# Performance work log

Hardware: AMD Instinct MI355X
Metric: run time of the kernel (lower is better)

## Reference

```python
import jax, jax.numpy as jnp
import numpy as np

B, L, C, K, NLEV, VOCAB, OUT = 32, 1024, 512, 2, 4, 128, 11


def setup_inputs() -> dict:
    key = jax.random.key(0)
    ks = jax.random.split(key, 8)
    x = jax.random.randint(ks[0], (B, L), 0, VOCAB, dtype=jnp.int32)
    mask = jax.random.randint(ks[1], (B, L), 0, 2).astype(jnp.bool_)
    emb = jax.random.uniform(ks[2], (VOCAB, C), minval=-0.5, maxval=0.5, dtype=jnp.float32)
    w1 = jax.random.normal(ks[3], (NLEV, C, C, K), dtype=jnp.float32) * 0.02
    b1 = jnp.zeros((NLEV, C), dtype=jnp.float32)
    w2 = jax.random.normal(ks[4], (NLEV, C, C, K), dtype=jnp.float32) * 0.02
    b2 = jnp.zeros((NLEV, C), dtype=jnp.float32)
    dec_w = jax.random.uniform(ks[5], (OUT, C), minval=-0.5, maxval=0.5, dtype=jnp.float32)
    dec_b = jnp.zeros((OUT,), dtype=jnp.float32)
    return dict(x=x, mask=mask, emb=emb, w1=w1, b1=b1, w2=w2, b2=b2, dec_w=dec_w, dec_b=dec_b)


def _causal_conv(h, w, b, dilation):
    # h: [B, C, L], w: [Cout, Cin, K]; left-pad (K-1)*d == conv+chomp in TCN
    pad = (w.shape[-1] - 1) * dilation
    out = jax.lax.conv_general_dilated(
        h, w, window_strides=(1,), padding=[(pad, 0)],
        rhs_dilation=(dilation,), dimension_numbers=("NCH", "OIH", "NCH"))
    return out + b[None, :, None]


def reference(x, mask, emb, w1, b1, w2, b2, dec_w, dec_b):
    h = emb[x].transpose(0, 2, 1)  # [B, C, L]
    for i in range(NLEV):  # fixed small number of TCN levels
        d = 2 ** i
        res = h
        h = jax.nn.relu(_causal_conv(h, w1[i], b1[i], d))
        h = jax.nn.relu(_causal_conv(h, w2[i], b2[i], d))
        h = jax.nn.relu(h + res)  # residual (in==out channels -> identity shortcut)
    y = jnp.einsum("bcl,oc->blo", h, dec_w) + dec_b  # [B, L, OUT]
    # mask-gather: original keeps only mask-true positions; zero others (jit-safe)
    return y * mask[..., None].astype(y.dtype)
```

## Files before the change

### kernel.cpp

```cpp
#include <hip/hip_runtime.h>
#include <stdint.h>

#define BB 32
#define LL 1024
#define CC 512
#define NN (BB * LL)
#define NLEVS 4
#define OUTD 11
#define LPAD 8
#define LROWS (LL + LPAD)

typedef __attribute__((ext_vector_type(8))) short bf16x8;
typedef __attribute__((ext_vector_type(4))) float f32x4;

static __device__ __forceinline__ unsigned short f2bf(float f) {
    union { float f; uint32_t u; } v; v.f = f;
    uint32_t u = v.u;
    uint32_t r = (u + 0x7fffu + ((u >> 16) & 1u)) >> 16;
    return (unsigned short)r;
}
static __device__ __forceinline__ float bf2f(unsigned short h) {
    union { uint32_t u; float f; } v; v.u = ((uint32_t)h) << 16;
    return v.f;
}

static __device__ __forceinline__ void llds16(const unsigned short* g, unsigned short* l) {
    __builtin_amdgcn_global_load_lds(
        (const __attribute__((address_space(1))) unsigned int*)g,
        (__attribute__((address_space(3))) unsigned int*)l, 16, 0, 0);
}

__global__ __launch_bounds__(256) void prep_kernel(
    const int* __restrict__ x, const float* __restrict__ emb,
    const float* __restrict__ w1, const float* __restrict__ w2,
    const float* __restrict__ dw,
    unsigned short* __restrict__ Hb0, unsigned short* __restrict__ Hb1,
    unsigned short* __restrict__ WpT, unsigned short* __restrict__ dwp)
{
    int b = blockIdx.x;
    if (b < 16384) {
        int e = b * 256 + threadIdx.x;
        int cv = e >> 19;
        int r = e & 524287;
        int j = r >> 12;
        int co = (r >> 3) & 511;
        int h = r & 7;
        int kidx = j * 8 + h;
        int k = (kidx < 512) ? 1 : 0;
        int ci = kidx & 511;
        int lvl = cv >> 1;
        const float* w = (cv & 1) ? w2 : w1;
        WpT[e] = f2bf(w[(((size_t)(lvl * 512 + co) * 512) + ci) * 2 + k]);
    } else if (b < 24576) {
        int t = (b - 16384) * 256 + threadIdx.x;
        int n = t >> 6;
        int c8 = (t & 63) * 8;
        int idx = x[n];
        const float* src = emb + (size_t)idx * CC + c8;
        float4 v0 = *(const float4*)src;
        float4 v1 = *(const float4*)(src + 4);
        ushort4 a, bb;
        a.x = f2bf(v0.x); a.y = f2bf(v0.y); a.z = f2bf(v0.z); a.w = f2bf(v0.w);
        bb.x = f2bf(v1.x); bb.y = f2bf(v1.y); bb.z = f2bf(v1.z); bb.w = f2bf(v1.w);
        int prow = (n >> 10) * LROWS + LPAD + (n & (LL - 1));
        unsigned short* dst = Hb0 + (size_t)prow * CC + c8;
        *(ushort4*)dst = a;
        *(ushort4*)(dst + 4) = bb;
    } else if (b < 24704) {
        int t = (b - 24576) * 256 + threadIdx.x;
        unsigned short* base = (t >> 14) ? Hb1 : Hb0;
        int rem = t & 16383;
        int p = rem >> 9;
        int q = rem & 511;
        size_t off = (size_t)p * (LROWS * CC) + (size_t)q * 8;
        *(uint4*)(base + off) = (uint4){0u, 0u, 0u, 0u};
    } else {
        int e = (b - 24704) * 256 + threadIdx.x;
        int jb = e >> 7;
        int o = (e >> 3) & 15;
        int j = e & 7;
        dwp[e] = f2bf((o < OUTD) ? dw[o * CC + jb * 8 + j] : 0.f);
    }
}

#define BUFH (17 * 512)
template <bool HAS_RES>
__global__ __launch_bounds__(256, 4) void conv_gemm(
    const unsigned short* __restrict__ Ain, const unsigned short* __restrict__ WpT,
    const float* __restrict__ bias, const unsigned short* __restrict__ resB,
    unsigned short* __restrict__ OutB, int d)
{
    __shared__ unsigned short sA[2 * BUFH];
    __shared__ int s_ready[8];
    __shared__ int s_done[8];

    const int tid = threadIdx.x;
    const int wave = tid >> 6, lane = tid & 63;

    const int bid = blockIdx.x;
    const int xcd = bid & 7;
    const int local = bid >> 3;
    const int cb = local >> 5;
    const int nb = xcd + 8 * (local & 31);
    const int co0 = cb * 128;
    const int n0 = nb * 128;

    const int rbase = (n0 >> 10) * LROWS + LPAD + (n0 & (LL - 1));
    const int wm = (wave >> 1) * 64;
    const int wn = (wave & 1) * 64;
    const int lm = lane & 15, quad = lane >> 4;

    const int r8 = lane >> 3;
    const int c8 = lane & 7;

    if (tid < 8) { s_ready[tid] = 0; s_done[tid] = 0; }
    __syncthreads();

    f32x4 acc[4][4];
#pragma unroll
    for (int i = 0; i < 4; ++i)
#pragma unroll
        for (int j = 0; j < 4; ++j) acc[i][j] = (f32x4){0.f, 0.f, 0.f, 0.f};

    auto issue = [&](int it) {
        const unsigned short* gA =
            Ain + (size_t)(rbase - 8 + r8) * CC + it * 64 + (c8 ^ r8) * 8;
        unsigned short* lbase = sA + (it & 1) * BUFH;
        for (int seg = wave; seg < 17; seg += 4)
            llds16(gA + (size_t)seg * 8 * CC, lbase + seg * 512);
    };
    auto spin4 = [&](int* p) {
        volatile int* vp = (volatile int*)p;
        while (*vp < 4) __builtin_amdgcn_s_sleep(1);
    };

    issue(0);

    for (int it = 0; it < 8; ++it) {
        if (it < 7) {
            if (it >= 1) spin4(&s_done[it - 1]);
            issue(it + 1);
            if (wave == 0) __builtin_amdgcn_s_waitcnt(0xF75);
            else           __builtin_amdgcn_s_waitcnt(0xF74);
        } else {
            __builtin_amdgcn_s_waitcnt(0xF70);
        }
        __asm__ volatile("" ::: "memory");
        if (lane == 0) atomicAdd(&s_ready[it], 1);
        spin4(&s_ready[it]);
        __asm__ volatile("" ::: "memory");

        const unsigned short* buf = sA + (it & 1) * BUFH;
        const int jb0 = it * 8;

        auto loadA = [&](int s, bf16x8* af) {
            const int t = s >> 1, ks = s & 1;
            const int shift = t ? d : 0;
            const int rowoff = 8 - shift + wm;
            const int key = (8 - shift + lm) & 7;
            const int cpos = ((ks * 4 + quad) ^ key);
#pragma unroll
            for (int mt = 0; mt < 4; ++mt)
                af[mt] = *(const bf16x8*)&buf[(rowoff + mt * 16 + lm) * 64 + cpos * 8];
        };
        auto loadB = [&](int s, bf16x8* bf) {
            const int t = s >> 1, ks = s & 1;
            const int jb = t * 64 + jb0 + ks * 4 + quad;
            const unsigned short* bbase = WpT + ((size_t)jb * 512 + co0 + wn + lm) * 8;
#pragma unroll
            for (int nt = 0; nt < 4; ++nt)
                bf[nt] = *(const bf16x8*)(bbase + (size_t)nt * 16 * 8);
        };

        bf16x8 afc[4], bfc[4], afn[4], bfn[4];
        loadA(0, afc);
        loadB(0, bfc);
#pragma unroll
        for (int s = 0; s < 4; ++s) {
            if (s < 3) { loadA(s + 1, afn); loadB(s + 1, bfn); }
#pragma unroll
            for (int mt = 0; mt < 4; ++mt)
#pragma unroll
                for (int nt = 0; nt < 4; ++nt)
                    acc[mt][nt] = __builtin_amdgcn_mfma_f32_16x16x32_bf16(
                        afc[mt], bfc[nt], acc[mt][nt], 0, 0, 0);
            if (s < 3) {
#pragma unroll
                for (int q2 = 0; q2 < 4; ++q2) { afc[q2] = afn[q2]; bfc[q2] = bfn[q2]; }
            }
        }

        __asm__ volatile("" ::: "memory");
        if (lane == 0) atomicAdd(&s_done[it], 1);
    }

    float bv[4];
#pragma unroll
    for (int nt = 0; nt < 4; ++nt) bv[nt] = bias[co0 + wn + nt * 16 + lm];

#pragma unroll
    for (int mt = 0; mt < 4; ++mt) {
        int prow0 = rbase + wm + mt * 16 + quad * 4;
#pragma unroll
        for (int nt = 0; nt < 4; ++nt) {
            int co = co0 + wn + nt * 16 + lm;
#pragma unroll
            for (int r = 0; r < 4; ++r) {
                size_t off = (size_t)(prow0 + r) * CC + co;
                float v = acc[mt][nt][r] + bv[nt];
                v = fmaxf(v, 0.f);
                if (HAS_RES) {
                    v += bf2f(resB[off]);
                    v = fmaxf(v, 0.f);
                }
                OutB[off] = f2bf(v);
            }
        }
    }
}

__global__ __launch_bounds__(256) void decode_kernel(
    const unsigned short* __restrict__ H, const unsigned short* __restrict__ dwp,
    const float* __restrict__ db, const int* __restrict__ mask,
    float* __restrict__ out)
{
    const int wave = threadIdx.x >> 6, lane = threadIdx.x & 63;
    const int lm = lane & 15, quad = lane >> 4;
    const int n0 = blockIdx.x * 64 + wave * 16;
    const int prow = ((n0 + lm) >> 10) * LROWS + LPAD + ((n0 + lm) & (LL - 1));

    f32x4 acc = (f32x4){0.f, 0.f, 0.f, 0.f};
#pragma unroll
    for (int ks = 0; ks < 16; ++ks) {
        bf16x8 af = *(const bf16x8*)&H[(size_t)prow * CC + ks * 32 + quad * 8];
        bf16x8 bf = *(const bf16x8*)&dwp[((size_t)(ks * 4 + quad) * 16 + lm) * 8];
        acc = __builtin_amdgcn_mfma_f32_16x16x32_bf16(af, bf, acc, 0, 0, 0);
    }

    if (lm < OUTD) {
        float bo = db[lm];
#pragma unroll
        for (int r = 0; r < 4; ++r) {
            int n = n0 + quad * 4 + r;
            float v = (mask[n] != 0) ? (acc[r] + bo) : 0.f;
            out[(size_t)n * OUTD + lm] = v;
        }
    }
}

extern "C" void kernel_launch(void* const* d_in, const int* in_sizes, int n_in,
                              void* d_out, int out_size, void* d_ws, size_t ws_size,
                              hipStream_t stream)
{
    const int* x = (const int*)d_in[0];
    const int* mask = (const int*)d_in[1];
    const float* emb = (const float*)d_in[2];
    const float* w1 = (const float*)d_in[3];
    const float* b1 = (const float*)d_in[4];
    const float* w2 = (const float*)d_in[5];
    const float* b2 = (const float*)d_in[6];
    const float* dw = (const float*)d_in[7];
    const float* db = (const float*)d_in[8];
    float* out = (float*)d_out;

    char* ws = (char*)d_ws;
    const size_t HBB = (size_t)BB * LROWS * CC * 2;
    unsigned short* Hb0 = (unsigned short*)ws;
    unsigned short* Hb1 = (unsigned short*)(ws + HBB);
    unsigned short* WpT = (unsigned short*)(ws + 2 * HBB);
    unsigned short* dwp = (unsigned short*)(ws + 2 * HBB + (size_t)NLEVS * 2 * CC * 1024 * 2);

    prep_kernel<<<24736, 256, 0, stream>>>(x, emb, w1, w2, dw, Hb0, Hb1, WpT, dwp);

    const int grid = (CC / 128) * (NN / 128);
    for (int i = 0; i < NLEVS; ++i) {
        int d = 1 << i;
        const unsigned short* W1 = WpT + (size_t)(i * 2 + 0) * CC * 1024;
        const unsigned short* W2 = WpT + (size_t)(i * 2 + 1) * CC * 1024;
        conv_gemm<false><<<grid, 256, 0, stream>>>(Hb0, W1, b1 + i * CC, nullptr, Hb1, d);
        conv_gemm<true><<<grid, 256, 0, stream>>>(Hb1, W2, b2 + i * CC, Hb0, Hb0, d);
    }
    decode_kernel<<<NN / 64, 256, 0, stream>>>(Hb0, dwp, db, mask, out);
}
```

Measured before the change: 379.8 us.

## Vectorize weight repack, prefetch B fragments before barrier, and widen decode tiles

The weight repack in the prep kernel now has each thread read 16 contiguous floats and write two 8-element bf16 vectors, one per tap, replacing scalar strided gathers and cutting prep blocks. The conv GEMM loads all B-weight fragments for an iteration from global memory before the LDS sync spin, so their latency overlaps the wait, at the cost of holding 16 extra vector registers. The decode kernel loads its weight fragments once into registers and processes two 16-row subtiles per wave, halving the grid.

```diff
diff --git a/kernel.cpp b/kernel.cpp
--- a/kernel.cpp
+++ b/kernel.cpp
@@ -38,21 +38,28 @@
     unsigned short* __restrict__ WpT, unsigned short* __restrict__ dwp)
 {
     int b = blockIdx.x;
-    if (b < 16384) {
-        int e = b * 256 + threadIdx.x;
-        int cv = e >> 19;
-        int r = e & 524287;
-        int j = r >> 12;
-        int co = (r >> 3) & 511;
-        int h = r & 7;
-        int kidx = j * 8 + h;
-        int k = (kidx < 512) ? 1 : 0;
-        int ci = kidx & 511;
+    if (b < 1024) {
+        int t = b * 256 + threadIdx.x;
+        int co = t & 511;
+        int jj = (t >> 9) & 63;
+        int cv = t >> 15;
         int lvl = cv >> 1;
         const float* w = (cv & 1) ? w2 : w1;
-        WpT[e] = f2bf(w[(((size_t)(lvl * 512 + co) * 512) + ci) * 2 + k]);
-    } else if (b < 24576) {
-        int t = (b - 16384) * 256 + threadIdx.x;
+        const float* src = w + ((size_t)(lvl * 512 + co) * 512 + jj * 8) * 2;
+        float4 f0 = ((const float4*)src)[0];
+        float4 f1 = ((const float4*)src)[1];
+        float4 f2 = ((const float4*)src)[2];
+        float4 f3 = ((const float4*)src)[3];
+        ushort4 t1a = {f2bf(f0.y), f2bf(f0.w), f2bf(f1.y), f2bf(f1.w)};
+        ushort4 t1b = {f2bf(f2.y), f2bf(f2.w), f2bf(f3.y), f2bf(f3.w)};
+        ushort4 t0a = {f2bf(f0.x), f2bf(f0.z), f2bf(f1.x), f2bf(f1.z)};
+        ushort4 t0b = {f2bf(f2.x), f2bf(f2.z), f2bf(f3.x), f2bf(f3.z)};
+        unsigned short* d1 = WpT + ((size_t)(cv * 128 + jj) * 512 + co) * 8;
+        unsigned short* d0 = WpT + ((size_t)(cv * 128 + jj + 64) * 512 + co) * 8;
+        *(ushort4*)d1 = t1a; *(ushort4*)(d1 + 4) = t1b;
+        *(ushort4*)d0 = t0a; *(ushort4*)(d0 + 4) = t0b;
+    } else if (b < 9216) {
+        int t = (b - 1024) * 256 + threadIdx.x;
         int n = t >> 6;
         int c8 = (t & 63) * 8;
         int idx = x[n];
@@ -66,8 +73,8 @@
         unsigned short* dst = Hb0 + (size_t)prow * CC + c8;
         *(ushort4*)dst = a;
         *(ushort4*)(dst + 4) = bb;
-    } else if (b < 24704) {
-        int t = (b - 24576) * 256 + threadIdx.x;
+    } else if (b < 9344) {
+        int t = (b - 9216) * 256 + threadIdx.x;
         unsigned short* base = (t >> 14) ? Hb1 : Hb0;
         int rem = t & 16383;
         int p = rem >> 9;
@@ -75,7 +82,7 @@
         size_t off = (size_t)p * (LROWS * CC) + (size_t)q * 8;
         *(uint4*)(base + off) = (uint4){0u, 0u, 0u, 0u};
     } else {
-        int e = (b - 24704) * 256 + threadIdx.x;
+        int e = (b - 9344) * 256 + threadIdx.x;
         int jb = e >> 7;
         int o = (e >> 3) & 15;
         int j = e & 7;
@@ -137,6 +144,17 @@
     issue(0);
 
     for (int it = 0; it < 8; ++it) {
+        bf16x8 ball[4][4];
+#pragma unroll
+        for (int s = 0; s < 4; ++s) {
+            const int t = s >> 1, ks = s & 1;
+            const int jb = t * 64 + it * 8 + ks * 4 + quad;
+            const unsigned short* bbase = WpT + ((size_t)jb * 512 + co0 + wn + lm) * 8;
+#pragma unroll
+            for (int nt = 0; nt < 4; ++nt)
+                ball[s][nt] = *(const bf16x8*)(bbase + (size_t)nt * 16 * 8);
+        }
+
         if (it < 7) {
             if (it >= 1) spin4(&s_done[it - 1]);
             issue(it + 1);
@@ -151,7 +169,6 @@
         __asm__ volatile("" ::: "memory");
 
         const unsigned short* buf = sA + (it & 1) * BUFH;
-        const int jb0 = it * 8;
 
         auto loadA = [&](int s, bf16x8* af) {
             const int t = s >> 1, ks = s & 1;
@@ -163,30 +180,21 @@
             for (int mt = 0; mt < 4; ++mt)
                 af[mt] = *(const bf16x8*)&buf[(rowoff + mt * 16 + lm) * 64 + cpos * 8];
         };
-        auto loadB = [&](int s, bf16x8* bf) {
-            const int t = s >> 1, ks = s & 1;
-            const int jb = t * 64 + jb0 + ks * 4 + quad;
-            const unsigned short* bbase = WpT + ((size_t)jb * 512 + co0 + wn + lm) * 8;
-#pragma unroll
-            for (int nt = 0; nt < 4; ++nt)
-                bf[nt] = *(const bf16x8*)(bbase + (size_t)nt * 16 * 8);
-        };
-
-        bf16x8 afc[4], bfc[4], afn[4], bfn[4];
+
+        bf16x8 afc[4], afn[4];
         loadA(0, afc);
-        loadB(0, bfc);
 #pragma unroll
         for (int s = 0; s < 4; ++s) {
-            if (s < 3) { loadA(s + 1, afn); loadB(s + 1, bfn); }
+            if (s < 3) loadA(s + 1, afn);
 #pragma unroll
             for (int mt = 0; mt < 4; ++mt)
 #pragma unroll
                 for (int nt = 0; nt < 4; ++nt)
                     acc[mt][nt] = __builtin_amdgcn_mfma_f32_16x16x32_bf16(
-                        afc[mt], bfc[nt], acc[mt][nt], 0, 0, 0);
+                        afc[mt], ball[s][nt], acc[mt][nt], 0, 0, 0);
             if (s < 3) {
 #pragma unroll
-                for (int q2 = 0; q2 < 4; ++q2) { afc[q2] = afn[q2]; bfc[q2] = bfn[q2]; }
+                for (int q2 = 0; q2 < 4; ++q2) afc[q2] = afn[q2];
             }
         }
 
@@ -226,24 +234,31 @@
 {
     const int wave = threadIdx.x >> 6, lane = threadIdx.x & 63;
     const int lm = lane & 15, quad = lane >> 4;
-    const int n0 = blockIdx.x * 64 + wave * 16;
-    const int prow = ((n0 + lm) >> 10) * LROWS + LPAD + ((n0 + lm) & (LL - 1));
-
-    f32x4 acc = (f32x4){0.f, 0.f, 0.f, 0.f};
-#pragma unroll
-    for (int ks = 0; ks < 16; ++ks) {
-        bf16x8 af = *(const bf16x8*)&H[(size_t)prow * CC + ks * 32 + quad * 8];
-        bf16x8 bf = *(const bf16x8*)&dwp[((size_t)(ks * 4 + quad) * 16 + lm) * 8];
-        acc = __builtin_amdgcn_mfma_f32_16x16x32_bf16(af, bf, acc, 0, 0, 0);
-    }
-
-    if (lm < OUTD) {
-        float bo = db[lm];
-#pragma unroll
-        for (int r = 0; r < 4; ++r) {
-            int n = n0 + quad * 4 + r;
-            float v = (mask[n] != 0) ? (acc[r] + bo) : 0.f;
-            out[(size_t)n * OUTD + lm] = v;
+
+    bf16x8 bfr[16];
+#pragma unroll
+    for (int ks = 0; ks < 16; ++ks)
+        bfr[ks] = *(const bf16x8*)&dwp[((size_t)(ks * 4 + quad) * 16 + lm) * 8];
+
+    const int base = blockIdx.x * 128 + wave * 32;
+#pragma unroll
+    for (int sub = 0; sub < 2; ++sub) {
+        int n0 = base + sub * 16;
+        int prow = ((n0 + lm) >> 10) * LROWS + LPAD + ((n0 + lm) & (LL - 1));
+        f32x4 acc = (f32x4){0.f, 0.f, 0.f, 0.f};
+#pragma unroll
+        for (int ks = 0; ks < 16; ++ks) {
+            bf16x8 af = *(const bf16x8*)&H[(size_t)prow * CC + ks * 32 + quad * 8];
+            acc = __builtin_amdgcn_mfma_f32_16x16x32_bf16(af, bfr[ks], acc, 0, 0, 0);
+        }
+        if (lm < OUTD) {
+            float bo = db[lm];
+#pragma unroll
+            for (int r = 0; r < 4; ++r) {
+                int n = n0 + quad * 4 + r;
+                float v = (mask[n] != 0) ? (acc[r] + bo) : 0.f;
+                out[(size_t)n * OUTD + lm] = v;
+            }
         }
     }
 }
@@ -270,7 +285,7 @@
     unsigned short* WpT = (unsigned short*)(ws + 2 * HBB);
     unsigned short* dwp = (unsigned short*)(ws + 2 * HBB + (size_t)NLEVS * 2 * CC * 1024 * 2);
 
-    prep_kernel<<<24736, 256, 0, stream>>>(x, emb, w1, w2, dw, Hb0, Hb1, WpT, dwp);
+    prep_kernel<<<9376, 256, 0, stream>>>(x, emb, w1, w2, dw, Hb0, Hb1, WpT, dwp);
 
     const int grid = (CC / 128) * (NN / 128);
     for (int i = 0; i < NLEVS; ++i) {
@@ -280,5 +295,5 @@
         conv_gemm<false><<<grid, 256, 0, stream>>>(Hb0, W1, b1 + i * CC, nullptr, Hb1, d);
         conv_gemm<true><<<grid, 256, 0, stream>>>(Hb1, W2, b2 + i * CC, Hb0, Hb0, d);
     }
-    decode_kernel<<<NN / 64, 256, 0, stream>>>(Hb0, dwp, db, mask, out);
-}
+    decode_kernel<<<NN / 128, 256, 0, stream>>>(Hb0, dwp, db, mask, out);
+}
```

Measured after the change: 773.3 us. +103.6%, slower.
